# Performance work log

Hardware: AMD Instinct MI355X
Metric: run time of the kernel (lower is better)

Reference implementation:

```python
import jax, jax.numpy as jnp
import numpy as np

# MalConv-style dims: byte vocab, tiny embed, wide stride-=kernel gated conv
B, T, V, E, C, K, S, N = 8, 1048576, 257, 8, 128, 512, 512, 64


def setup_inputs() -> dict:
    key = jax.random.key(0)
    k1, k2, k3, k4 = jax.random.split(key, 4)
    x = jax.random.randint(k1, (B, T), 0, V, dtype=jnp.int32)
    emb = jax.random.normal(k2, (V, E), dtype=jnp.float32) * 0.02
    fan = 1.0 / np.sqrt(E * K)
    w1 = jax.random.normal(k3, (C, E, K), dtype=jnp.float32) * fan
    w2 = jax.random.normal(k4, (C, E, K), dtype=jnp.float32) * fan
    b1 = jnp.zeros((C,), jnp.float32)
    b2 = jnp.zeros((C,), jnp.float32)
    return {"x": x, "emb": emb, "w1": w1, "b1": b1, "w2": w2, "b2": b2}


def reference(x, emb, w1, b1, w2, b2):
    # preprocess: byte embedding -> (B, E, T)
    z = emb[x].transpose(0, 2, 1)
    dn = ("NCH", "OIH", "NCH")
    # GatedConvolution: c1 * sigmoid(c2), valid conv, stride S -> (B, C, L)
    c1 = jax.lax.conv_general_dilated(z, w1, (S,), "VALID", dimension_numbers=dn) + b1[None, :, None]
    c2 = jax.lax.conv_general_dilated(z, w2, (S,), "VALID", dimension_numbers=dn) + b2[None, :, None]
    g = c1 * jax.nn.sigmoid(c2)  # (B, C, L)
    L = g.shape[-1]
    # input-space position of each conv output window; patch assignment
    pos = jnp.arange(L, dtype=jnp.int32) * S
    patch_size = -(-T // N)  # ceil(T / num_patches)
    seg = jnp.clip(pos // patch_size, 0, N - 1)  # (L,)
    # per-patch max-over-time, per channel: segment_max over the L axis
    gl = g.transpose(2, 0, 1).reshape(L, B * C)  # (L, B*C)
    mv = jax.ops.segment_max(gl, seg, num_segments=N)  # (N, B*C)
    max_vals = mv.reshape(N, B, C).transpose(1, 0, 2)  # (B, N, C)
    return max_vals
```

## Files before the change

### kernel.cpp

```cpp
#include <hip/hip_runtime.h>
#include <hip/hip_bf16.h>
#include <math.h>


typedef __bf16 bf16x8 __attribute__((ext_vector_type(8)));
typedef float  f32x4  __attribute__((ext_vector_type(4)));

#define WS_WP_OFF   0u
#define WS_EMB_OFF  (2u << 20)
#define WS_XP_OFF   (4u << 20)
#define WS_C_OFF    (24u << 20)

__device__ __forceinline__ void load_lds16(const void* g, void* l) {
    __builtin_amdgcn_global_load_lds(
        (const __attribute__((address_space(1))) void*)g,
        (__attribute__((address_space(3))) void*)l,
        16, 0, 0);
}

__device__ __forceinline__ unsigned short f2bf(float f) {
    unsigned u = __builtin_bit_cast(unsigned, f);
    return (unsigned short)((u + 0x7fffu + ((u >> 16) & 1u)) >> 16);
}
__device__ __forceinline__ float bflo(unsigned u) {
    return __builtin_bit_cast(float, u << 16);
}
__device__ __forceinline__ float bfhi(unsigned u) {
    return __builtin_bit_cast(float, u & 0xffff0000u);
}

__global__ void prep_kernel(const float* __restrict__ w1,
                            const float* __restrict__ w2,
                            const float* __restrict__ emb,
                            const int* __restrict__ x,
                            uint4* __restrict__ Wp4,
                            __bf16* __restrict__ embp,
                            unsigned short* __restrict__ xp) {
    __shared__ __align__(16) char smem[256 * 136 * 2];
    int bid = blockIdx.x, tid = threadIdx.x;
    if (bid >= 64 && bid < 320) {
        unsigned short* lds = (unsigned short*)smem;
        int xbid = bid - 64;
        int mt = xbid >> 2, kh = xbid & 3;
        const long src0 = (long)mt * 131072 + kh * 128;
#pragma unroll
        for (int i = 0; i < 32; ++i) {
            int f = i * 256 + tid;
            int row = f >> 5, c = (f & 31) * 4;
            int4 v = *(const int4*)(x + src0 + (long)row * 512 + c);
            ushort4 s;
            s.x = (unsigned short)v.x; s.y = (unsigned short)v.y;
            s.z = (unsigned short)v.z; s.w = (unsigned short)v.w;
            *(ushort4*)&lds[row * 136 + c] = s;
        }
        __syncthreads();
        unsigned short* dst = xp + (size_t)xbid * 32768;
#pragma unroll
        for (int i = 0; i < 32; ++i) {
            int jc = i * 256 + tid;
            int rg = jc & 3, lane = (jc >> 2) & 63, wv = (jc >> 8) & 3, st = jc >> 10;
            int q = lane >> 4, nl = lane & 15;
            int row = wv * 64 + rg * 16 + nl;
            int cb = st * 16 + q;
            ushort4 s;
            s.x = lds[row * 136 + cb];
            s.y = lds[row * 136 + cb + 4];
            s.z = lds[row * 136 + cb + 8];
            s.w = lds[row * 136 + cb + 12];
            *(ushort4*)&dst[jc * 4] = s;
        }
    } else if (bid < 64) {
        __bf16* lds = (__bf16*)smem;
        int sg = bid & 31, nt = bid >> 5;
        const float* wsrc = nt ? w2 : w1;
#pragma unroll
        for (int i = 0; i < 16; ++i) {
            int g = i * 256 + tid;
            int j4 = g & 3, pair = g >> 2;
            int e = pair & 7, cl = pair >> 3;
            float4 v = *(const float4*)(wsrc + cl * 4096 + e * 512 + sg * 16 + j4 * 4);
            float vv[4] = {v.x, v.y, v.z, v.w};
#pragma unroll
            for (int jj = 0; jj < 4; ++jj)
                lds[(cl * 16 + j4 * 4 + jj) * 8 + e] = (__bf16)vv[jj];
        }
        __syncthreads();
        const uint4* l4 = (const uint4*)lds;
#pragma unroll
        for (int it = 0; it < 8; ++it) {
            int j = it * 256 + tid;
            int n = j & 127, q = (j >> 7) & 3, tt = (j >> 9) & 3;
            Wp4[bid * 2048 + j] = l4[n * 16 + tt * 4 + q];
        }
    } else {
        for (int i = tid; i < 2056; i += 256) embp[i] = (__bf16)emb[i];
    }
}

__global__ __launch_bounds__(256, 2)
void gemm_kernel(const unsigned short* __restrict__ xp,
                 const __bf16* __restrict__ Wp,
                 const uint4* __restrict__ embp,
                 unsigned short* __restrict__ Cbuf) {
    __shared__ uint4 ldsB[2][2048];
    __shared__ uint4 embl[257];

    const int tid = threadIdx.x;
    const int wv = tid >> 6, lane = tid & 63;
    const int q = lane >> 4, nl = lane & 15;

    for (int i = tid; i < 257; i += 256) embl[i] = embp[i];

    const int bid = blockIdx.x;
    const int mt = bid >> 3, nt = bid & 1, kh = (bid >> 1) & 3;
    const int m0 = mt << 8;

    const char* WpBase = (const char*)Wp + (size_t)(nt * 32 + kh * 8) * 32768;
    const unsigned short* xpS = xp + (size_t)(mt * 4 + kh) * 32768 + (wv * 64 + lane) * 16;

    {
        const char* src = WpBase + tid * 16;
        char* dstl = (char*)&ldsB[0][0] + tid * 16;
#pragma unroll
        for (int i = 0; i < 8; ++i) load_lds16(src + i * 4096, dstl + i * 4096);
    }
    uint4 xa = *(const uint4*)(xpS);
    uint4 xb = *(const uint4*)(xpS + 8);
    __syncthreads();

    f32x4 acc[4][8] = {};

    for (int st = 0; st < 8; ++st) {
        const int buf = st & 1;
        uint4 xa_n = xa, xb_n = xb;
        if (st < 7) {
            const char* src = WpBase + (size_t)(st + 1) * 32768 + tid * 16;
            char* dstl = (char*)&ldsB[buf ^ 1][0] + tid * 16;
#pragma unroll
            for (int i = 0; i < 8; ++i) load_lds16(src + i * 4096, dstl + i * 4096);
            const unsigned short* xn = xpS + (size_t)(st + 1) * 4096;
            xa_n = *(const uint4*)(xn);
            xb_n = *(const uint4*)(xn + 8);
        }
        const unsigned int u[8] = {xa.x, xa.y, xa.z, xa.w, xb.x, xb.y, xb.z, xb.w};
#pragma unroll
        for (int tt = 0; tt < 4; ++tt) {
            bf16x8 a[4];
#pragma unroll
            for (int rg = 0; rg < 4; ++rg) {
                unsigned int w = u[rg * 2 + (tt >> 1)];
                int idx = (tt & 1) ? (int)(w >> 16) : (int)(w & 0xffffu);
                a[rg] = *reinterpret_cast<const bf16x8*>(&embl[idx]);
            }
            const char* Bb = (const char*)&ldsB[buf][0] + (((tt * 4 + q) * 128 + nl) << 4);
#pragma unroll
            for (int nf = 0; nf < 8; ++nf) {
                bf16x8 b = *reinterpret_cast<const bf16x8*>(Bb + nf * 256);
#pragma unroll
                for (int rg = 0; rg < 4; ++rg)
                    acc[rg][nf] = __builtin_amdgcn_mfma_f32_16x16x32_bf16(a[rg], b, acc[rg][nf], 0, 0, 0);
            }
        }
        xa = xa_n; xb = xb_n;
        __syncthreads();
    }

    unsigned short* Cp = Cbuf + (size_t)kh * 4194304;
#pragma unroll
    for (int rg = 0; rg < 4; ++rg) {
        int rowb = m0 + wv * 64 + rg * 16 + q * 4;
#pragma unroll
        for (int nf = 0; nf < 8; ++nf) {
            int col = nt * 128 + nf * 16 + nl;
#pragma unroll
            for (int i = 0; i < 4; ++i)
                Cp[(size_t)(rowb + i) * 256 + col] = f2bf(acc[rg][nf][i]);
        }
    }
}

__global__ void reduce_kernel(const unsigned short* __restrict__ Cbuf,
                              const float* __restrict__ b1,
                              const float* __restrict__ b2,
                              float* __restrict__ out) {
    __shared__ float smC[32 * 256];
    __shared__ f32x4 smM[8 * 32];
    int tid = threadIdx.x, gp = blockIdx.x;
    size_t base = (size_t)gp * 32 * 256;
#pragma unroll
    for (int i = 0; i < 4; ++i) {
        int ch = i * 256 + tid;
        int row = ch >> 5, c8 = ch & 31;
        float s[8] = {};
#pragma unroll
        for (int kh = 0; kh < 4; ++kh) {
            uint4 v = *(const uint4*)(Cbuf + (size_t)kh * 4194304 + base + row * 256 + c8 * 8);
            s[0] += bflo(v.x); s[1] += bfhi(v.x);
            s[2] += bflo(v.y); s[3] += bfhi(v.y);
            s[4] += bflo(v.z); s[5] += bfhi(v.z);
            s[6] += bflo(v.w); s[7] += bfhi(v.w);
        }
        float* d = &smC[row * 256 + c8 * 8];
        *(f32x4*)d       = f32x4{s[0], s[1], s[2], s[3]};
        *(f32x4*)(d + 4) = f32x4{s[4], s[5], s[6], s[7]};
    }
    __syncthreads();
    int c4 = tid & 31, rgp = tid >> 5;
    f32x4 bb1 = *(const f32x4*)(b1 + c4 * 4);
    f32x4 bb2 = *(const f32x4*)(b2 + c4 * 4);
    f32x4 m;
    m[0] = m[1] = m[2] = m[3] = -INFINITY;
#pragma unroll
    for (int r = 0; r < 4; ++r) {
        int row = rgp * 4 + r;
        f32x4 a = *(const f32x4*)&smC[row * 256 + c4 * 4];
        f32x4 b = *(const f32x4*)&smC[row * 256 + 128 + c4 * 4];
#pragma unroll
        for (int j = 0; j < 4; ++j) {
            float g = (a[j] + bb1[j]) * (1.0f / (1.0f + __expf(-(b[j] + bb2[j]))));
            m[j] = fmaxf(m[j], g);
        }
    }
    smM[rgp * 32 + c4] = m;
    __syncthreads();
    if (tid < 32) {
        f32x4 mm = smM[tid];
#pragma unroll
        for (int r = 1; r < 8; ++r) {
            f32x4 v = smM[r * 32 + tid];
#pragma unroll
            for (int j = 0; j < 4; ++j) mm[j] = fmaxf(mm[j], v[j]);
        }
        *(f32x4*)(out + gp * 128 + tid * 4) = mm;
    }
}

extern "C" void kernel_launch(void* const* d_in, const int* in_sizes, int n_in,
                              void* d_out, int out_size, void* d_ws, size_t ws_size,
                              hipStream_t stream) {
    const int*   x   = (const int*)d_in[0];
    const float* emb = (const float*)d_in[1];
    const float* w1  = (const float*)d_in[2];
    const float* b1  = (const float*)d_in[3];
    const float* w2  = (const float*)d_in[4];
    const float* b2  = (const float*)d_in[5];
    float* out = (float*)d_out;

    char* ws = (char*)d_ws;
    __bf16*         Wp    = (__bf16*)(ws + WS_WP_OFF);
    __bf16*         embp  = (__bf16*)(ws + WS_EMB_OFF);
    unsigned short* xpp   = (unsigned short*)(ws + WS_XP_OFF);
    unsigned short* Cbuf  = (unsigned short*)(ws + WS_C_OFF);

    prep_kernel<<<321, 256, 0, stream>>>(w1, w2, emb, x, (uint4*)Wp, embp, xpp);
    gemm_kernel<<<512, 256, 0, stream>>>(xpp, Wp, (const uint4*)embp, Cbuf);
    reduce_kernel<<<512, 256, 0, stream>>>(Cbuf, b1, b2, out);
}
```

Before: 128.6 us.

## Load GEMM weight fragments directly from global into registers, drop LDS staging

Rewrites the weight prepack so each lane's MFMA B fragment sits contiguously in global memory, then has the GEMM read B straight into registers instead of double-buffering through LDS with global_load_lds. This removes the per-stage block barrier and the LDS traffic for B, and frees LDS, which could allow higher occupancy. In exchange every wave fetches its own copy of B from L2/global, so the four waves of a block make redundant global reads, and there is less explicit prefetch to hide latency.

```diff
diff --git a/kernel.cpp b/kernel.cpp
--- a/kernel.cpp
+++ b/kernel.cpp
@@ -10,13 +10,6 @@
 #define WS_EMB_OFF  (2u << 20)
 #define WS_XP_OFF   (4u << 20)
 #define WS_C_OFF    (24u << 20)
-
-__device__ __forceinline__ void load_lds16(const void* g, void* l) {
-    __builtin_amdgcn_global_load_lds(
-        (const __attribute__((address_space(1))) void*)g,
-        (__attribute__((address_space(3))) void*)l,
-        16, 0, 0);
-}
 
 __device__ __forceinline__ unsigned short f2bf(float f) {
     unsigned u = __builtin_bit_cast(unsigned, f);
@@ -71,8 +64,9 @@
         }
     } else if (bid < 64) {
         __bf16* lds = (__bf16*)smem;
-        int sg = bid & 31, nt = bid >> 5;
-        const float* wsrc = nt ? w2 : w1;
+        int sg = bid & 31, ns = bid >> 5;
+        int kh = sg >> 3, st = sg & 7;
+        const float* wsrc = ns ? w2 : w1;
 #pragma unroll
         for (int i = 0; i < 16; ++i) {
             int g = i * 256 + tid;
@@ -89,8 +83,9 @@
 #pragma unroll
         for (int it = 0; it < 8; ++it) {
             int j = it * 256 + tid;
-            int n = j & 127, q = (j >> 7) & 3, tt = (j >> 9) & 3;
-            Wp4[bid * 2048 + j] = l4[n * 16 + tt * 4 + q];
+            int nl = j & 15, q = (j >> 4) & 3, nf = (j >> 6) & 7, tt = j >> 9;
+            int cl = nf * 16 + nl;
+            Wp4[ns * 65536 + kh * 16384 + st * 2048 + j] = l4[cl * 16 + tt * 4 + q];
         }
     } else {
         for (int i = tid; i < 2056; i += 256) embp[i] = (__bf16)emb[i];
@@ -99,10 +94,9 @@
 
 __global__ __launch_bounds__(256, 2)
 void gemm_kernel(const unsigned short* __restrict__ xp,
-                 const __bf16* __restrict__ Wp,
+                 const uint4* __restrict__ Wp4,
                  const uint4* __restrict__ embp,
                  unsigned short* __restrict__ Cbuf) {
-    __shared__ uint4 ldsB[2][2048];
     __shared__ uint4 embl[257];
 
     const int tid = threadIdx.x;
@@ -110,34 +104,23 @@
     const int q = lane >> 4, nl = lane & 15;
 
     for (int i = tid; i < 257; i += 256) embl[i] = embp[i];
+    __syncthreads();
 
     const int bid = blockIdx.x;
-    const int mt = bid >> 3, nt = bid & 1, kh = (bid >> 1) & 3;
+    const int mt = bid >> 3, ns = bid & 1, kh = (bid >> 1) & 3;
     const int m0 = mt << 8;
 
-    const char* WpBase = (const char*)Wp + (size_t)(nt * 32 + kh * 8) * 32768;
+    const uint4* WpS = Wp4 + ns * 65536 + kh * 16384 + lane;
     const unsigned short* xpS = xp + (size_t)(mt * 4 + kh) * 32768 + (wv * 64 + lane) * 16;
 
-    {
-        const char* src = WpBase + tid * 16;
-        char* dstl = (char*)&ldsB[0][0] + tid * 16;
-#pragma unroll
-        for (int i = 0; i < 8; ++i) load_lds16(src + i * 4096, dstl + i * 4096);
-    }
     uint4 xa = *(const uint4*)(xpS);
     uint4 xb = *(const uint4*)(xpS + 8);
-    __syncthreads();
 
     f32x4 acc[4][8] = {};
 
     for (int st = 0; st < 8; ++st) {
-        const int buf = st & 1;
         uint4 xa_n = xa, xb_n = xb;
         if (st < 7) {
-            const char* src = WpBase + (size_t)(st + 1) * 32768 + tid * 16;
-            char* dstl = (char*)&ldsB[buf ^ 1][0] + tid * 16;
-#pragma unroll
-            for (int i = 0; i < 8; ++i) load_lds16(src + i * 4096, dstl + i * 4096);
             const unsigned short* xn = xpS + (size_t)(st + 1) * 4096;
             xa_n = *(const uint4*)(xn);
             xb_n = *(const uint4*)(xn + 8);
@@ -145,6 +128,10 @@
         const unsigned int u[8] = {xa.x, xa.y, xa.z, xa.w, xb.x, xb.y, xb.z, xb.w};
 #pragma unroll
         for (int tt = 0; tt < 4; ++tt) {
+            const uint4* Bp = WpS + (st * 4 + tt) * 512;
+            uint4 braw[8];
+#pragma unroll
+            for (int nf = 0; nf < 8; ++nf) braw[nf] = Bp[nf * 64];
             bf16x8 a[4];
 #pragma unroll
             for (int rg = 0; rg < 4; ++rg) {
@@ -152,17 +139,15 @@
                 int idx = (tt & 1) ? (int)(w >> 16) : (int)(w & 0xffffu);
                 a[rg] = *reinterpret_cast<const bf16x8*>(&embl[idx]);
             }
-            const char* Bb = (const char*)&ldsB[buf][0] + (((tt * 4 + q) * 128 + nl) << 4);
 #pragma unroll
             for (int nf = 0; nf < 8; ++nf) {
-                bf16x8 b = *reinterpret_cast<const bf16x8*>(Bb + nf * 256);
+                bf16x8 b = __builtin_bit_cast(bf16x8, braw[nf]);
 #pragma unroll
                 for (int rg = 0; rg < 4; ++rg)
                     acc[rg][nf] = __builtin_amdgcn_mfma_f32_16x16x32_bf16(a[rg], b, acc[rg][nf], 0, 0, 0);
             }
         }
         xa = xa_n; xb = xb_n;
-        __syncthreads();
     }
 
     unsigned short* Cp = Cbuf + (size_t)kh * 4194304;
@@ -171,7 +156,7 @@
         int rowb = m0 + wv * 64 + rg * 16 + q * 4;
 #pragma unroll
         for (int nf = 0; nf < 8; ++nf) {
-            int col = nt * 128 + nf * 16 + nl;
+            int col = ns * 128 + nf * 16 + nl;
 #pragma unroll
             for (int i = 0; i < 4; ++i)
                 Cp[(size_t)(rowb + i) * 256 + col] = f2bf(acc[rg][nf][i]);
@@ -247,12 +232,12 @@
     float* out = (float*)d_out;
 
     char* ws = (char*)d_ws;
-    __bf16*         Wp    = (__bf16*)(ws + WS_WP_OFF);
+    uint4*          Wp4   = (uint4*)(ws + WS_WP_OFF);
     __bf16*         embp  = (__bf16*)(ws + WS_EMB_OFF);
     unsigned short* xpp   = (unsigned short*)(ws + WS_XP_OFF);
     unsigned short* Cbuf  = (unsigned short*)(ws + WS_C_OFF);
 
-    prep_kernel<<<321, 256, 0, stream>>>(w1, w2, emb, x, (uint4*)Wp, embp, xpp);
-    gemm_kernel<<<512, 256, 0, stream>>>(xpp, Wp, (const uint4*)embp, Cbuf);
+    prep_kernel<<<321, 256, 0, stream>>>(w1, w2, emb, x, Wp4, embp, xpp);
+    gemm_kernel<<<512, 256, 0, stream>>>(xpp, Wp4, (const uint4*)embp, Cbuf);
     reduce_kernel<<<512, 256, 0, stream>>>(Cbuf, b1, b2, out);
 }
```

After: 156.6 us. 1.22x slower.
